# Kernel tuning notes

Hardware: AMD Instinct MI355X
Metric: run time of the kernel (lower is better)

## Reference

```python
import jax, jax.numpy as jnp
import numpy as np

HID = 2048      # hidden_size
H = 16          # num_heads == num_kv_heads (stack in fwd forces MHA)
DH = HID // H   # head_size = 128
QKV = 3 * H * DH  # 6144
THETA = 10000.0
EPS = 1e-5      # flash-attn RMSNorm default eps
B, L = 4, 2048


def setup_inputs() -> dict:
    key = jax.random.key(0)
    k1, k2, k3 = jax.random.split(key, 3)
    hidden_states = jax.random.normal(k1, (B, L, HID), dtype=jnp.float32)
    # weights stored as (in, out); scaled like a typical init so activations stay sane
    W_qkvg = jax.random.normal(k2, (HID, QKV + HID), dtype=jnp.float32) * 0.02
    W_out = jax.random.normal(k3, (HID, HID), dtype=jnp.float32) * 0.02
    return {"hidden_states": hidden_states, "W_qkvg": W_qkvg, "W_out": W_out}


def _rmsnorm(x):
    # elementwise_affine=False: pure rms normalization over head dim
    return x * jax.lax.rsqrt(jnp.mean(x * x, axis=-1, keepdims=True) + EPS)


def _rope(x, seqlen_offset=0):
    # x: (B, L, H, DH), non-interleaved (GPT-NeoX style rotate-half)
    half = DH // 2
    inv_freq = 1.0 / (THETA ** (jnp.arange(half, dtype=jnp.float32) * 2.0 / DH))
    pos = jnp.arange(seqlen_offset, seqlen_offset + x.shape[1], dtype=jnp.float32)
    ang = pos[:, None] * inv_freq[None, :]                  # (L, half)
    cos = jnp.cos(ang)[None, :, None, :]                    # (1,L,1,half)
    sin = jnp.sin(ang)[None, :, None, :]
    x1, x2 = x[..., :half], x[..., half:]
    return jnp.concatenate([x1 * cos - x2 * sin, x1 * sin + x2 * cos], axis=-1)


def _attention_forward(hidden_states, W_qkvg, W_out):
    b, l, _ = hidden_states.shape
    proj = hidden_states @ W_qkvg                           # (B,L,QKV+HID)
    qkv_flat, gate = proj[..., :QKV], proj[..., QKV:]
    gate = jax.nn.sigmoid(gate)
    qkv = qkv_flat.reshape(b, l, 3 * H, DH)
    q, k, v = qkv[:, :, :H], qkv[:, :, H:2 * H], qkv[:, :, 2 * H:]
    q = _rope(_rmsnorm(q))
    k = _rope(_rmsnorm(k))
    # causal softmax attention (math of flash_attn_func)
    scores = jnp.einsum('blhd,bmhd->bhlm', q, k) / np.sqrt(DH).astype(np.float32)
    causal = jnp.tril(jnp.ones((l, l), dtype=bool))
    scores = jnp.where(causal[None, None], scores, jnp.finfo(scores.dtype).min)
    attn = jax.nn.softmax(scores, axis=-1)
    out = jnp.einsum('bhlm,bmhd->blhd', attn, v).reshape(b, l, HID)
    out = out * gate
    return out @ W_out


def reference(hidden_states, W_qkvg, W_out):
    return _attention_forward(hidden_states, W_qkvg, W_out)
```

## Files before the change

### kernel.cpp

```cpp
#include <hip/hip_runtime.h>


typedef __attribute__((ext_vector_type(8))) short bf16x8;
typedef __attribute__((ext_vector_type(4))) float f32x4;
typedef __attribute__((ext_vector_type(4))) unsigned short us4;

#if __has_builtin(__builtin_amdgcn_exp2f)
#define EXP2(x) __builtin_amdgcn_exp2f(x)
#else
#define EXP2(x) exp2f(x)
#endif

__device__ __forceinline__ unsigned short f2bf(float f) {
    unsigned int x = __float_as_uint(f);
    unsigned int r = x + 0x7fffu + ((x >> 16) & 1u);
    return (unsigned short)(r >> 16);
}
__device__ __forceinline__ unsigned short f2bf_fast(float f) {
    return (unsigned short)((__float_as_uint(f) + 0x8000u) >> 16);
}
__device__ __forceinline__ float bf2f(unsigned short u) {
    return __uint_as_float(((unsigned int)u) << 16);
}

__device__ __forceinline__ void gll16(const unsigned short* g, unsigned short* l) {
    __builtin_amdgcn_global_load_lds(
        (const __attribute__((address_space(1))) unsigned int*)g,
        (__attribute__((address_space(3))) unsigned int*)l, 16, 0, 0);
}

__device__ __forceinline__ void barx() {
    asm volatile("" ::: "memory");
    __builtin_amdgcn_s_barrier();
    asm volatile("" ::: "memory");
}
#define LGKM0() asm volatile("s_waitcnt lgkmcnt(0)" ::: "memory")
#define VM6()   asm volatile("s_waitcnt vmcnt(6)" ::: "memory")
#define VM4()   asm volatile("s_waitcnt vmcnt(4)" ::: "memory")
#define VM0()   asm volatile("s_waitcnt vmcnt(0)" ::: "memory")

__global__ __launch_bounds__(256) void cvt_bf16(const float* __restrict__ in,
                                                unsigned short* __restrict__ out) {
    int i = blockIdx.x * 256 + threadIdx.x;
    float4 v = ((const float4*)in)[i];
    us4 r;
    r[0] = f2bf(v.x); r[1] = f2bf(v.y); r[2] = f2bf(v.z); r[3] = f2bf(v.w);
    ((us4*)out)[i] = r;
}

__global__ __launch_bounds__(256) void transpose_cvt(const float* __restrict__ in,
                                                     unsigned short* __restrict__ out,
                                                     int R, int C) {
    __shared__ float t[32][33];
    int c0 = blockIdx.x * 32, r0 = blockIdx.y * 32;
    int tx = threadIdx.x, ty = threadIdx.y;
#pragma unroll
    for (int i = 0; i < 4; i++)
        t[ty + i * 8][tx] = in[(size_t)(r0 + ty + i * 8) * C + c0 + tx];
    __syncthreads();
#pragma unroll
    for (int i = 0; i < 4; i++)
        out[(size_t)(c0 + ty + i * 8) * R + r0 + tx] = f2bf(t[tx][ty + i * 8]);
}

__device__ __forceinline__ void gemm256_core(const unsigned short* __restrict__ A,
                                             const unsigned short* __restrict__ Bt,
                                             int K, int rowA0, int colB0,
                                             unsigned short* sm,
                                             f32x4 acc[8][4]) {
    const int tid = threadIdx.x;
    const int w = tid >> 6, lane = tid & 63;
    const int quad = lane >> 4, l15 = lane & 15;
    const int wm = w >> 2, wn = w & 3;
    const int lr = lane >> 3;
    const int lc = ((lane & 7) ^ lr) * 8;
    const int NT = K >> 6;

    const unsigned short* pA = A  + (size_t)(rowA0 + w * 16 + lr) * K + lc;
    const unsigned short* pB = Bt + (size_t)(colB0 + w * 16 + lr) * K + lc;
    unsigned short* lw = sm + w * 16 * 64;

#define STAGE(tt, isB, h)                                                       \
    do {                                                                        \
        const unsigned short* gp_ = ((isB) ? pB : pA) +                         \
            (size_t)(h) * 128 * K + (size_t)(tt) * 64;                          \
        unsigned short* lp_ = lw + (((tt) & 1) * 4 + (isB) * 2 + (h)) * 8192;   \
        gll16(gp_, lp_);                                                        \
        gll16(gp_ + (size_t)8 * K, lp_ + 8 * 64);                               \
    } while (0)

    STAGE(0, 1, 0); STAGE(0, 1, 1); STAGE(0, 0, 0); STAGE(0, 0, 1);
    STAGE(1, 1, 0); STAGE(1, 1, 1); STAGE(1, 0, 0);
    VM6();
    barx();

    for (int t = 0; t < NT; ++t) {
        const unsigned short* Asl = sm + ((t & 1) * 4 + wm) * 8192;
        const unsigned short* Bsl = sm + ((t & 1) * 4 + 2 + (wn >> 1)) * 8192;
        bf16x8 bfrag[4][2];
#pragma unroll
        for (int q = 0; q < 4; ++q) {
            if (q == 0) {
#pragma unroll
                for (int nj = 0; nj < 4; ++nj)
#pragma unroll
                    for (int kk = 0; kk < 2; ++kk) {
                        int r = (wn & 1) * 64 + nj * 16 + l15;
                        bfrag[nj][kk] = *(const bf16x8*)&Bsl[r * 64 +
                            (((kk * 4 + quad) ^ (r & 7)) * 8)];
                    }
            }
            bf16x8 afr[2][2];
#pragma unroll
            for (int mi = 0; mi < 2; ++mi)
#pragma unroll
                for (int kk = 0; kk < 2; ++kk) {
                    int r = q * 32 + mi * 16 + l15;
                    afr[mi][kk] = *(const bf16x8*)&Asl[r * 64 +
                        (((kk * 4 + quad) ^ (r & 7)) * 8)];
                }
            if (q == 0)      { if (t + 1 < NT) STAGE(t + 1, 0, 1); }
            else if (q == 1) { if (t + 2 < NT) STAGE(t + 2, 1, 0); }
            else if (q == 2) { if (t + 2 < NT) STAGE(t + 2, 1, 1); }
            else {
                if (t + 2 < NT)      { STAGE(t + 2, 0, 0); VM6(); }
                else if (t + 1 < NT) { VM0(); }
            }
            barx();
            LGKM0();
            __builtin_amdgcn_s_setprio(1);
#pragma unroll
            for (int mi = 0; mi < 2; ++mi)
#pragma unroll
                for (int nj = 0; nj < 4; ++nj)
#pragma unroll
                    for (int kk = 0; kk < 2; ++kk)
                        acc[q * 2 + mi][nj] = __builtin_amdgcn_mfma_f32_16x16x32_bf16(
                            afr[mi][kk], bfrag[nj][kk], acc[q * 2 + mi][nj], 0, 0, 0);
            __builtin_amdgcn_s_setprio(0);
            barx();
        }
    }
#undef STAGE
}

__global__ __launch_bounds__(512) void gemm_qkvg(const unsigned short* __restrict__ A,
                                                 const unsigned short* __restrict__ Bt,
                                                 unsigned short* __restrict__ Qb,
                                                 unsigned short* __restrict__ Kb,
                                                 unsigned short* __restrict__ Vt,
                                                 unsigned short* __restrict__ Gb) {
    __shared__ unsigned short sm[8 * 8192];
    f32x4 acc[8][4];
    f32x4 z = {0.f, 0.f, 0.f, 0.f};
#pragma unroll
    for (int i = 0; i < 8; i++)
#pragma unroll
        for (int j = 0; j < 4; j++) acc[i][j] = z;

    const int g = blockIdx.y * 32 + blockIdx.x;
    const int gs = (g & 7) * 128 + (g >> 3);
    const int bx = gs & 31, by = gs >> 5;
    const int rowA0 = by * 256, colB0 = bx * 256;
    gemm256_core(A, Bt, 2048, rowA0, colB0, sm, acc);

    const int tid = threadIdx.x, w = tid >> 6, lane = tid & 63;
    const int quad = lane >> 4, l15 = lane & 15;
    const int wm = w >> 2, wn = w & 3;
    const int sec = colB0 >> 11;
    const int hbase = (colB0 & 2047) >> 7;

    if (sec == 2) {
#pragma unroll
        for (int mi = 0; mi < 8; ++mi)
#pragma unroll
            for (int nj = 0; nj < 4; ++nj)
#pragma unroll
                for (int i = 0; i < 4; ++i) {
                    int ll = wm * 128 + mi * 16 + quad * 4 + i;
                    int c  = wn * 64 + nj * 16 + l15;
                    int hh = c >> 7, d = c & 127;
                    sm[hh * 32768 + d * 256 + (((ll >> 3) ^ (d & 31)) * 8) + (ll & 7)] =
                        f2bf(acc[mi][nj][i]);
                }
        __syncthreads();
        const int b_ = rowA0 >> 11, l0 = rowA0 & 2047;
        const int d = tid >> 2, part = tid & 3;
#pragma unroll
        for (int hh = 0; hh < 2; ++hh) {
            unsigned short* drow = Vt +
                ((size_t)(b_ * 16 + hbase + hh) * 128 + d) * 2048 + l0 + part * 64;
#pragma unroll
            for (int j = 0; j < 8; ++j) {
                int chunk = part * 8 + j;
                *(bf16x8*)(drow + j * 8) =
                    *(const bf16x8*)&sm[hh * 32768 + d * 256 + ((chunk ^ (d & 31)) * 8)];
            }
        }
    } else if (sec == 3) {
#pragma unroll
        for (int mi = 0; mi < 8; ++mi)
#pragma unroll
            for (int nj = 0; nj < 4; ++nj)
#pragma unroll
                for (int i = 0; i < 4; ++i) {
                    int rowg = rowA0 + wm * 128 + mi * 16 + quad * 4 + i;
                    int c = wn * 64 + nj * 16 + l15;
                    int h = hbase + (c >> 7), d = c & 127;
                    float gv = 1.f / (1.f + __expf(-acc[mi][nj][i]));
                    Gb[((size_t)rowg << 11) + h * 128 + d] = f2bf(gv);
                }
    } else {
        unsigned short* dst = (sec == 0) ? Qb : Kb;
#pragma unroll
        for (int mi = 0; mi < 8; ++mi)
#pragma unroll
            for (int nj = 0; nj < 4; ++nj)
#pragma unroll
                for (int i = 0; i < 4; ++i) {
                    int rowg = rowA0 + wm * 128 + mi * 16 + quad * 4 + i;
                    int c = wn * 64 + nj * 16 + l15;
                    int h = hbase + (c >> 7), d = c & 127;
                    int b_ = rowg >> 11, l_ = rowg & 2047;
                    dst[(((size_t)(b_ * 16 + h) * 2048 + l_) << 7) + d] =
                        f2bf(acc[mi][nj][i]);
                }
    }
}

__global__ __launch_bounds__(512) void gemm_out(const unsigned short* __restrict__ A,
                                                const unsigned short* __restrict__ Bt,
                                                float* __restrict__ C) {
    __shared__ unsigned short sm[8 * 8192];
    f32x4 acc[8][4];
    f32x4 z = {0.f, 0.f, 0.f, 0.f};
#pragma unroll
    for (int i = 0; i < 8; i++)
#pragma unroll
        for (int j = 0; j < 4; j++) acc[i][j] = z;

    const int g = blockIdx.y * 8 + blockIdx.x;
    const int gs = (g & 7) * 32 + (g >> 3);
    const int bx = gs & 7, by = gs >> 3;
    const int rowA0 = by * 256, colB0 = bx * 256;
    gemm256_core(A, Bt, 2048, rowA0, colB0, sm, acc);

    const int tid = threadIdx.x, w = tid >> 6, lane = tid & 63;
    const int quad = lane >> 4, l15 = lane & 15;
    const int wm = w >> 2, wn = w & 3;
#pragma unroll
    for (int mi = 0; mi < 8; ++mi)
#pragma unroll
        for (int nj = 0; nj < 4; ++nj)
#pragma unroll
            for (int i = 0; i < 4; ++i) {
                int rowg = rowA0 + wm * 128 + mi * 16 + quad * 4 + i;
                int col = colB0 + wn * 64 + nj * 16 + l15;
                C[(size_t)rowg * 2048 + col] = acc[mi][nj][i];
            }
}

__global__ __launch_bounds__(256) void rmsnorm_rope(unsigned short* __restrict__ Qp,
                                                    unsigned short* __restrict__ Kp) {
    unsigned short* X = blockIdx.y ? Kp : Qp;
    const int tid = threadIdx.x;
    const int wv = tid >> 6, lane = tid & 63;
    const int rgrp = lane >> 4;
    const int l16 = lane & 15;
    const int sub = l16 >> 3, l8 = l16 & 7;
    const int row = blockIdx.x * 16 + wv * 4 + rgrp;
    unsigned short* p = X + (size_t)row * 128 + sub * 64 + l8 * 8;
    const int pos = row & 2047;

    bf16x8 v = *(const bf16x8*)p;
    float x[8];
    float ss = 0.f;
#pragma unroll
    for (int j = 0; j < 8; j++) {
        x[j] = bf2f((unsigned short)v[j]);
        ss += x[j] * x[j];
    }
#pragma unroll
    for (int off = 8; off >= 1; off >>= 1) ss += __shfl_xor(ss, off, 16);
    const float r = rsqrtf(ss * (1.f / 128.f) + 1e-5f);

    float xs[8], xp[8];
#pragma unroll
    for (int j = 0; j < 8; j++) xs[j] = x[j] * r;
#pragma unroll
    for (int j = 0; j < 8; j++) xp[j] = __shfl_xor(xs[j], 8, 16);

    const float sgn = sub ? 1.f : -1.f;
    bf16x8 o;
#pragma unroll
    for (int j = 0; j < 8; j++) {
        int k = l8 * 8 + j;
        float inv = exp2f(-(float)k * (13.287712379549449f / 64.f));
        float ang = (float)pos * inv;
        float sn, cs;
        sincosf(ang, &sn, &cs);
        o[j] = (short)f2bf(xs[j] * cs + xp[j] * (sgn * sn));
    }
    *(bf16x8*)p = o;
}

__global__ __launch_bounds__(512) void fa_kernel(const unsigned short* __restrict__ Q,
                                                 const unsigned short* __restrict__ K,
                                                 const unsigned short* __restrict__ Vt,
                                                 const unsigned short* __restrict__ G,
                                                 unsigned short* __restrict__ Og) {
    __shared__ unsigned short Ks[2][64 * 128];
    __shared__ unsigned short Vs[2][128 * 64];
    __shared__ unsigned short Ps[256 * 32];
    const int g = blockIdx.x;
    const int bh = (g & 7) | ((g >> 6) << 3);
    const int qc = (g >> 3) & 7;
    const int tid = threadIdx.x, w = tid >> 6, lane = tid & 63;
    const int quad = lane >> 4, l15 = lane & 15;
    const int sw = l15 & 7;
    const int qrow0 = qc * 256 + w * 32;
    const float CS = 0.12751740395609812f;

    bf16x8 qf[2][4];
#pragma unroll
    for (int mi = 0; mi < 2; mi++)
#pragma unroll
        for (int kt = 0; kt < 4; kt++)
            qf[mi][kt] = *(const bf16x8*)(Q + ((size_t)bh * 2048 + qrow0 + mi * 16 + l15) * 128
                                             + kt * 32 + quad * 8);

    f32x4 o[2][8];
    f32x4 z = {0.f, 0.f, 0.f, 0.f};
#pragma unroll
    for (int mi = 0; mi < 2; mi++)
#pragma unroll
        for (int nj = 0; nj < 8; nj++) o[mi][nj] = z;
    float rowsum[2][4];
#pragma unroll
    for (int mi = 0; mi < 2; mi++)
#pragma unroll
        for (int i = 0; i < 4; i++) rowsum[mi][i] = 0.f;

    const unsigned short* Kbase = K + (size_t)bh * 2048 * 128;
    const unsigned short* Vtb   = Vt + (size_t)bh * 128 * 2048;

    const int krow = lane >> 4, kc = lane & 15;
    const int vrow = lane >> 3, vc = lane & 7;

#define STAGE_KV(jj, buf)                                                        \
    do {                                                                         \
        _Pragma("unroll")                                                        \
        for (int i_ = 0; i_ < 2; i_++) {                                         \
            int r0_ = w * 8 + i_ * 4;                                            \
            int row_ = r0_ + krow;                                               \
            int cs_ = (kc & 8) | ((kc & 7) ^ (row_ & 7));                        \
            gll16(Kbase + (size_t)((jj) * 64 + row_) * 128 + cs_ * 8,            \
                  &Ks[buf][r0_ * 128]);                                          \
        }                                                                        \
        _Pragma("unroll")                                                        \
        for (int i_ = 0; i_ < 2; i_++) {                                         \
            int r0_ = w * 16 + i_ * 8;                                           \
            int row_ = r0_ + vrow;                                               \
            gll16(Vtb + (size_t)row_ * 2048 + (jj) * 64 + ((vc ^ (row_ & 7)) * 8), \
                  &Vs[buf][r0_ * 64]);                                           \
        }                                                                        \
    } while (0)

    const int pr0 = w * 32 + l15, pr1 = pr0 + 16;
    const int pk0 = (pr0 >> 1) & 3, pk1 = (pr1 >> 1) & 3;

    const int NJ = 4 * (qc + 1);

    STAGE_KV(0, 0);

    for (int j = 0; j < NJ; j++) {
        const int cur = j & 1;
        if (j + 1 < NJ) { STAGE_KV(j + 1, cur ^ 1); VM4(); }
        else            { VM0(); }
        barx();

        if (j * 64 < qrow0 + 32) {
            f32x4 s[2][4];
#pragma unroll
            for (int mi = 0; mi < 2; mi++)
#pragma unroll
                for (int nj = 0; nj < 4; nj++) s[mi][nj] = z;
            __builtin_amdgcn_s_setprio(1);
#pragma unroll
            for (int kt = 0; kt < 4; kt++)
#pragma unroll
                for (int nj = 0; nj < 4; nj++) {
                    bf16x8 bfr = *(const bf16x8*)&Ks[cur][(nj * 16 + l15) * 128 +
                                                         (((kt * 4 + quad) ^ sw) * 8)];
                    s[0][nj] = __builtin_amdgcn_mfma_f32_16x16x32_bf16(qf[0][kt], bfr, s[0][nj], 0, 0, 0);
                    s[1][nj] = __builtin_amdgcn_mfma_f32_16x16x32_bf16(qf[1][kt], bfr, s[1][nj], 0, 0, 0);
                }
            __builtin_amdgcn_s_setprio(0);

            const bool diag = (j * 64 + 63 > qrow0);
#pragma unroll
            for (int hh = 0; hh < 2; hh++) {
#pragma unroll
                for (int mi = 0; mi < 2; mi++)
#pragma unroll
                    for (int njh = 0; njh < 2; njh++) {
                        const int nj = hh * 2 + njh;
#pragma unroll
                        for (int i = 0; i < 4; i++) {
                            float pp = EXP2(s[mi][nj][i] * CS);
                            int row_l = mi * 16 + quad * 4 + i;
                            if (diag) {
                                int col_g = j * 64 + nj * 16 + l15;
                                if (col_g > qrow0 + row_l) pp = 0.f;
                            }
                            rowsum[mi][i] += pp;
                            int row = w * 32 + row_l;
                            int kv = njh * 16 + l15;
                            Ps[row * 32 + ((((kv >> 3) ^ ((row >> 1) & 3)) * 8)) + (kv & 7)] =
                                f2bf_fast(pp);
                        }
                    }
                bf16x8 a0 = *(const bf16x8*)&Ps[pr0 * 32 + ((quad ^ pk0) * 8)];
                bf16x8 a1 = *(const bf16x8*)&Ps[pr1 * 32 + ((quad ^ pk1) * 8)];
                __builtin_amdgcn_s_setprio(1);
#pragma unroll
                for (int nj = 0; nj < 8; nj++) {
                    bf16x8 bfr = *(const bf16x8*)&Vs[cur][(nj * 16 + l15) * 64 +
                                                          (((hh * 4 + quad) ^ sw) * 8)];
                    o[0][nj] = __builtin_amdgcn_mfma_f32_16x16x32_bf16(a0, bfr, o[0][nj], 0, 0, 0);
                    o[1][nj] = __builtin_amdgcn_mfma_f32_16x16x32_bf16(a1, bfr, o[1][nj], 0, 0, 0);
                }
                __builtin_amdgcn_s_setprio(0);
            }
        }
        barx();
    }
#undef STAGE_KV

    const int b_ = bh >> 4, h = bh & 15;
#pragma unroll
    for (int mi = 0; mi < 2; mi++)
#pragma unroll
        for (int i = 0; i < 4; i++) {
            float t = rowsum[mi][i];
#pragma unroll
            for (int off = 1; off < 16; off <<= 1) t += __shfl_xor(t, off, 16);
            float rl = 1.f / t;
            int l_ = qrow0 + mi * 16 + quad * 4 + i;
#pragma unroll
            for (int nj = 0; nj < 8; nj++) {
                int d = nj * 16 + l15;
                size_t gi = ((size_t)(b_ * 2048 + l_) * 2048) + h * 128 + d;
                Og[gi] = f2bf(o[mi][nj][i] * rl * bf2f(G[gi]));
            }
        }
}

extern "C" void kernel_launch(void* const* d_in, const int* in_sizes, int n_in,
                              void* d_out, int out_size, void* d_ws, size_t ws_size,
                              hipStream_t stream) {
    const float* X  = (const float*)d_in[0];
    const float* Wq = (const float*)d_in[1];
    const float* Wo = (const float*)d_in[2];
    float* out = (float*)d_out;

    char* ws = (char*)d_ws;
    const size_t SZ = 33554432ull;
    unsigned short* Xb  = (unsigned short*)(ws);
    unsigned short* Wqt = (unsigned short*)(ws + SZ);
    unsigned short* Wot = (unsigned short*)(ws + 2 * SZ);
    unsigned short* Qb  = (unsigned short*)(ws + 2 * SZ + 8388608ull);
    unsigned short* Kb  = (unsigned short*)(ws + 3 * SZ + 8388608ull);
    unsigned short* Vt  = (unsigned short*)(ws + 4 * SZ + 8388608ull);
    unsigned short* Gb  = (unsigned short*)(ws + 5 * SZ + 8388608ull);
    unsigned short* OG  = Xb;

    cvt_bf16<<<16384, 256, 0, stream>>>(X, Xb);
    transpose_cvt<<<dim3(256, 64), dim3(32, 8), 0, stream>>>(Wq, Wqt, 2048, 8192);
    transpose_cvt<<<dim3(64, 64),  dim3(32, 8), 0, stream>>>(Wo, Wot, 2048, 2048);

    gemm_qkvg<<<dim3(32, 32), 512, 0, stream>>>(Xb, Wqt, Qb, Kb, Vt, Gb);

    rmsnorm_rope<<<dim3(8192, 2), 256, 0, stream>>>(Qb, Kb);

    fa_kernel<<<512, 512, 0, stream>>>(Qb, Kb, Vt, Gb, OG);

    gemm_out<<<dim3(8, 32), 512, 0, stream>>>(OG, Wot, out);
}
```

Before: 692.7 us.

## Software-pipeline LDS fragment reads against MFMAs and schedule heavy causal blocks first

The shared GEMM core now double-buffers A and B register fragments, so it reads the next quarter's A fragments, and the next tile's B fragments, from LDS while the current MFMAs run. The loop is unrolled by two to ping-pong the B fragment buffers. This is meant to hide LDS read latency behind matrix math, at the cost of more registers. Separately, the flash-attention kernel reverses the query-chunk order so that blocks with the most causal work launch first, which should improve tail load balance.

Result: slower. 955.1 us (+37.9%).

```diff
diff --git a/kernel.cpp b/kernel.cpp
--- a/kernel.cpp
+++ b/kernel.cpp
@@ -80,6 +80,9 @@
     const unsigned short* pB = Bt + (size_t)(colB0 + w * 16 + lr) * K + lc;
     unsigned short* lw = sm + w * 16 * 64;
 
+    bf16x8 bfA[4][2], bfB[4][2];
+    bf16x8 af[2][2][2];
+
 #define STAGE(tt, isB, h)                                                       \
     do {                                                                        \
         const unsigned short* gp_ = ((isB) ? pB : pA) +                         \
@@ -89,58 +92,92 @@
         gll16(gp_ + (size_t)8 * K, lp_ + 8 * 64);                               \
     } while (0)
 
+#define RD_A(par, Asl_, qq)                                                     \
+    _Pragma("unroll")                                                           \
+    for (int mi = 0; mi < 2; ++mi)                                              \
+    _Pragma("unroll")                                                           \
+    for (int kk = 0; kk < 2; ++kk) {                                            \
+        int r = (qq) * 32 + mi * 16 + l15;                                      \
+        af[par][mi][kk] = *(const bf16x8*)&(Asl_)[r * 64 +                      \
+            (((kk * 4 + quad) ^ (r & 7)) * 8)];                                 \
+    }
+
+#define RD_B(dstB, Bsl_)                                                        \
+    _Pragma("unroll")                                                           \
+    for (int nj = 0; nj < 4; ++nj)                                              \
+    _Pragma("unroll")                                                           \
+    for (int kk = 0; kk < 2; ++kk) {                                            \
+        int r = (wn & 1) * 64 + nj * 16 + l15;                                  \
+        dstB[nj][kk] = *(const bf16x8*)&(Bsl_)[r * 64 +                         \
+            (((kk * 4 + quad) ^ (r & 7)) * 8)];                                 \
+    }
+
+#define MM(qpar, Bu, qq)                                                        \
+    __builtin_amdgcn_s_setprio(1);                                              \
+    _Pragma("unroll")                                                           \
+    for (int mi = 0; mi < 2; ++mi)                                              \
+    _Pragma("unroll")                                                           \
+    for (int nj = 0; nj < 4; ++nj)                                              \
+    _Pragma("unroll")                                                           \
+    for (int kk = 0; kk < 2; ++kk)                                              \
+        acc[(qq) * 2 + mi][nj] = __builtin_amdgcn_mfma_f32_16x16x32_bf16(       \
+            af[qpar][mi][kk], Bu[nj][kk], acc[(qq) * 2 + mi][nj], 0, 0, 0);     \
+    __builtin_amdgcn_s_setprio(0);
+
+#define TILE(t, Bu, Bn)                                                         \
+    {                                                                           \
+        const unsigned short* Asl = sm + (((t) & 1) * 4 + wm) * 8192;           \
+                                                                        \
+        if ((t) + 1 < NT) STAGE((t) + 1, 0, 1);                                 \
+        barx(); LGKM0();                                                        \
+        RD_A(1, Asl, 1);                                                        \
+        MM(0, Bu, 0);                                                           \
+        barx();                                                                 \
+                                                                        \
+        if ((t) + 2 < NT) STAGE((t) + 2, 1, 0);                                 \
+        barx(); LGKM0();                                                        \
+        RD_A(0, Asl, 2);                                                        \
+        MM(1, Bu, 1);                                                           \
+        barx();                                                                 \
+                                                                        \
+        if ((t) + 2 < NT) STAGE((t) + 2, 1, 1);                                 \
+        barx(); LGKM0();                                                        \
+        RD_A(1, Asl, 3);                                                        \
+        MM(0, Bu, 2);                                                           \
+        barx();                                                                 \
+                                                                        \
+        if ((t) + 2 < NT)      { STAGE((t) + 2, 0, 0); VM6(); }                 \
+        else if ((t) + 1 < NT) { VM0(); }                                       \
+        barx(); LGKM0();                                                        \
+        if ((t) + 1 < NT) {                                                     \
+            const unsigned short* Asn = sm + ((((t) + 1) & 1) * 4 + wm) * 8192; \
+            const unsigned short* Bsn = sm + ((((t) + 1) & 1) * 4 + 2 +         \
+                                              (wn >> 1)) * 8192;                \
+            RD_B(Bn, Bsn);                                                      \
+            RD_A(0, Asn, 0);                                                    \
+        }                                                                       \
+        MM(1, Bu, 3);                                                           \
+        barx();                                                                 \
+    }
+
     STAGE(0, 1, 0); STAGE(0, 1, 1); STAGE(0, 0, 0); STAGE(0, 0, 1);
     STAGE(1, 1, 0); STAGE(1, 1, 1); STAGE(1, 0, 0);
     VM6();
     barx();
-
-    for (int t = 0; t < NT; ++t) {
-        const unsigned short* Asl = sm + ((t & 1) * 4 + wm) * 8192;
-        const unsigned short* Bsl = sm + ((t & 1) * 4 + 2 + (wn >> 1)) * 8192;
-        bf16x8 bfrag[4][2];
-#pragma unroll
-        for (int q = 0; q < 4; ++q) {
-            if (q == 0) {
-#pragma unroll
-                for (int nj = 0; nj < 4; ++nj)
-#pragma unroll
-                    for (int kk = 0; kk < 2; ++kk) {
-                        int r = (wn & 1) * 64 + nj * 16 + l15;
-                        bfrag[nj][kk] = *(const bf16x8*)&Bsl[r * 64 +
-                            (((kk * 4 + quad) ^ (r & 7)) * 8)];
-                    }
-            }
-            bf16x8 afr[2][2];
-#pragma unroll
-            for (int mi = 0; mi < 2; ++mi)
-#pragma unroll
-                for (int kk = 0; kk < 2; ++kk) {
-                    int r = q * 32 + mi * 16 + l15;
-                    afr[mi][kk] = *(const bf16x8*)&Asl[r * 64 +
-                        (((kk * 4 + quad) ^ (r & 7)) * 8)];
-                }
-            if (q == 0)      { if (t + 1 < NT) STAGE(t + 1, 0, 1); }
-            else if (q == 1) { if (t + 2 < NT) STAGE(t + 2, 1, 0); }
-            else if (q == 2) { if (t + 2 < NT) STAGE(t + 2, 1, 1); }
-            else {
-                if (t + 2 < NT)      { STAGE(t + 2, 0, 0); VM6(); }
-                else if (t + 1 < NT) { VM0(); }
-            }
-            barx();
-            LGKM0();
-            __builtin_amdgcn_s_setprio(1);
-#pragma unroll
-            for (int mi = 0; mi < 2; ++mi)
-#pragma unroll
-                for (int nj = 0; nj < 4; ++nj)
-#pragma unroll
-                    for (int kk = 0; kk < 2; ++kk)
-                        acc[q * 2 + mi][nj] = __builtin_amdgcn_mfma_f32_16x16x32_bf16(
-                            afr[mi][kk], bfrag[nj][kk], acc[q * 2 + mi][nj], 0, 0, 0);
-            __builtin_amdgcn_s_setprio(0);
-            barx();
-        }
-    }
+    {
+        const unsigned short* Asl0 = sm + wm * 8192;
+        const unsigned short* Bsl0 = sm + (2 + (wn >> 1)) * 8192;
+        RD_B(bfA, Bsl0);
+        RD_A(0, Asl0, 0);
+    }
+    for (int tt = 0; tt < NT; tt += 2) {
+        TILE(tt, bfA, bfB);
+        TILE(tt + 1, bfB, bfA);
+    }
+#undef TILE
+#undef MM
+#undef RD_B
+#undef RD_A
 #undef STAGE
 }
 
@@ -314,7 +351,7 @@
     __shared__ unsigned short Ps[256 * 32];
     const int g = blockIdx.x;
     const int bh = (g & 7) | ((g >> 6) << 3);
-    const int qc = (g >> 3) & 7;
+    const int qc = 7 - ((g >> 3) & 7);
     const int tid = threadIdx.x, w = tid >> 6, lane = tid & 63;
     const int quad = lane >> 4, l15 = lane & 15;
     const int sw = l15 & 7;
```
